# Performance work log

Hardware: AMD Instinct MI355X
Metric: run time of the kernel (lower is better)

The kernel has to match this reference:

```python
import jax, jax.numpy as jnp
import numpy as np

B, S, HD, NH, AH, F = 64, 256, 512, 8, 256, 2
DH = HD // NH          # item/pos head dim = 64
DA = AH // NH          # attribute head dim = 32
EPS = 1e-12


def setup_inputs() -> dict:
    key = jax.random.key(0)
    ks = iter(jax.random.split(key, 32))
    rn = lambda shape, s=1.0: jax.random.normal(next(ks), shape, dtype=jnp.float32) * s
    w = 0.02
    return {
        "input_tensor": rn((B, S, HD)),
        "attribute_table": rn((B, S, 1, AH)),
        "position_embedding": rn((B, S, HD)),
        "Wq": rn((HD, HD), w), "bq": jnp.zeros((HD,), jnp.float32),
        "Wk": rn((HD, HD), w), "bk": jnp.zeros((HD,), jnp.float32),
        "Wv": rn((HD, HD), w), "bv": jnp.zeros((HD,), jnp.float32),
        "Wqp": rn((HD, HD), w), "bqp": jnp.zeros((HD,), jnp.float32),
        "Wkp": rn((HD, HD), w), "bkp": jnp.zeros((HD,), jnp.float32),
        "Wqa": rn((F, AH, AH), w), "bqa": jnp.zeros((F, AH), jnp.float32),
        "Wka": rn((F, AH, AH), w), "bka": jnp.zeros((F, AH), jnp.float32),
        "fw1": rn((S, S), w), "fb1": jnp.zeros((S,), jnp.float32),
        "fw2": rn((1, S), w), "fb2": jnp.zeros((1,), jnp.float32),
        "Wd": rn((HD, HD), w), "bd": jnp.zeros((HD,), jnp.float32),
        "gamma": jnp.ones((HD,), jnp.float32),
        "beta": jnp.zeros((HD,), jnp.float32),
    }


def _split_heads(x, nh):
    b, s, h = x.shape
    return x.reshape(b, s, nh, h // nh).transpose(0, 2, 1, 3)  # [B,H,S,d]


def reference(input_tensor, attribute_table, position_embedding,
              Wq, bq, Wk, bk, Wv, bv, Wqp, bqp, Wkp, bkp,
              Wqa, bqa, Wka, bka, fw1, fb1, fw2, fb2,
              Wd, bd, gamma, beta):
    q = _split_heads(input_tensor @ Wq.T + bq, NH)
    k = _split_heads(input_tensor @ Wk.T + bk, NH)
    v = _split_heads(input_tensor @ Wv.T + bv, NH)
    qp = _split_heads(position_embedding @ Wqp.T + bqp, NH)
    kp = _split_heads(position_embedding @ Wkp.T + bkp, NH)

    item_scores = jnp.einsum('bhqd,bhkd->bhqk', q, k)
    pos_scores = jnp.einsum('bhqd,bhkd->bhqk', qp, kp)

    attr = attribute_table.squeeze(-2)                       # [B,S,AH]
    qa = jnp.einsum('bsc,foc->fbso', attr, Wqa) + bqa[:, None, None, :]
    ka = jnp.einsum('bsc,foc->fbso', attr, Wka) + bka[:, None, None, :]
    qa = qa.reshape(F, B, S, NH, DA).transpose(0, 1, 3, 2, 4)  # [F,B,H,S,da]
    ka = ka.reshape(F, B, S, NH, DA).transpose(0, 1, 3, 2, 4)
    attr_scores = jnp.einsum('fbhqd,fbhkd->fbhqk', qa, ka)
    attr_scores = attr_scores.transpose(1, 2, 3, 0, 4)         # [B,H,S,F,S]

    # gate fusion (VanillaAttention over the F+2 score sources)
    stacked = jnp.concatenate(
        [attr_scores, item_scores[..., None, :], pos_scores[..., None, :]],
        axis=-2)                                               # [B,H,S,F+2,S]
    energy = jnp.maximum(stacked @ fw1.T + fb1, 0.0) @ fw2.T + fb2
    gate_w = jax.nn.softmax(energy.squeeze(-1), axis=-1)        # [B,H,S,F+2]
    scores = jnp.sum(stacked * gate_w[..., None], axis=-2)      # [B,H,S,S]

    scores = scores / np.sqrt(DH).astype(np.float32)
    probs = jax.nn.softmax(scores, axis=-1)
    ctx = jnp.einsum('bhqk,bhkd->bhqd', probs, v)
    ctx = ctx.transpose(0, 2, 1, 3).reshape(B, S, HD)

    h = ctx @ Wd.T + bd
    x = h + input_tensor
    mu = jnp.mean(x, axis=-1, keepdims=True)
    var = jnp.mean(jnp.square(x - mu), axis=-1, keepdims=True)
    return gamma * (x - mu) / jnp.sqrt(var + EPS) + beta
```

## Files before the change

### kernel.cpp

```cpp
#include <hip/hip_runtime.h>

typedef unsigned short u16;
typedef unsigned int   u32;
typedef __bf16 bf16x8 __attribute__((ext_vector_type(8)));
typedef float  f32x4  __attribute__((ext_vector_type(4)));
typedef u16    u16x4  __attribute__((ext_vector_type(4)));
typedef u16    u16x8  __attribute__((ext_vector_type(8)));

#define BB 64
#define SS 256
#define HDIM 512
#define NHEAD 8
#define BS (BB*SS)
#define NBH 512

__device__ __forceinline__ u16 f2bf(float f){
    u32 u = __builtin_bit_cast(u32, f);
    u32 r = u + 0x7FFFu + ((u>>16)&1u);
    return (u16)(r>>16);
}
__device__ __forceinline__ float bf2f(u16 u){
    return __builtin_bit_cast(float, (u32)u<<16);
}
__device__ __forceinline__ void gload16(const void* g, void* l){
    __builtin_amdgcn_global_load_lds(
        (const __attribute__((address_space(1))) void*)g,
        (__attribute__((address_space(3))) void*)l, 16, 0, 0);
}

__device__ __forceinline__ size_t zrow(int bh, int s){
    return ((size_t)bh*256 + s)*384;
}

__global__ __launch_bounds__(256) void cvt_k(const float* __restrict__ s,
                                             u16* __restrict__ d, int n8)
{
    int i = blockIdx.x*256 + threadIdx.x;
    const int stride = gridDim.x*256;
    for (; i < n8; i += stride) {
        f32x4 a = ((const f32x4*)s)[i*2];
        f32x4 b = ((const f32x4*)s)[i*2+1];
        u16x8 o = { f2bf(a[0]),f2bf(a[1]),f2bf(a[2]),f2bf(a[3]),
                    f2bf(b[0]),f2bf(b[1]),f2bf(b[2]),f2bf(b[3]) };
        ((u16x8*)d)[i] = o;
    }
}

__global__ __launch_bounds__(256) void cvtW_k(
    const float* __restrict__ Wq,  const float* __restrict__ Wk,
    const float* __restrict__ Wv,  const float* __restrict__ Wqp,
    const float* __restrict__ Wkp, const float* __restrict__ Wqa,
    const float* __restrict__ Wka, const float* __restrict__ Wd,
    u16* __restrict__ dst)
{
    const int i = blockIdx.x*256 + threadIdx.x;
    const float* s; u16* d; int local;
    if (i < 163840) {
        const int seg = i >> 15; local = i & 32767;
        s = seg==0?Wq:seg==1?Wk:seg==2?Wv:seg==3?Wqp:Wkp;
        d = dst + (size_t)seg*262144;
    } else if (i < 196608) {
        const int j = i - 163840; const int seg = j >> 14; local = j & 16383;
        s = seg ? Wka : Wqa;
        d = dst + 1310720 + (size_t)seg*131072;
    } else {
        local = i - 196608;
        s = Wd; d = dst + 1572864;
    }
    f32x4 a = ((const f32x4*)s)[local*2];
    f32x4 b = ((const f32x4*)s)[local*2+1];
    u16x8 o = { f2bf(a[0]),f2bf(a[1]),f2bf(a[2]),f2bf(a[3]),
                f2bf(b[0]),f2bf(b[1]),f2bf(b[2]),f2bf(b[3]) };
    ((u16x8*)d)[local] = o;
}

__global__ __launch_bounds__(64) void prep_fw1(const float* __restrict__ fw1,
                                               u16* __restrict__ fw1b)
{
    const int row = blockIdx.x;
    const int c0  = threadIdx.x * 4;
    float4 v = *(const float4*)(fw1 + (size_t)row*256 + c0);
    u16x4 pk = { f2bf(v.x), f2bf(v.y), f2bf(v.z), f2bf(v.w) };
    *(u16x4*)((char*)fw1b + (size_t)row*512 + ((c0*2) ^ ((row&7)<<4))) = pk;
}

template<int OUTMODE, int BBF16>
__global__ __launch_bounds__(256,2) void gemm128(
    const u16* __restrict__ A, const void* __restrict__ Bv,
    void* __restrict__ o0, void* __restrict__ o1, void* __restrict__ o2,
    const float* __restrict__ b0, const float* __restrict__ b1,
    const float* __restrict__ b2, const float* __restrict__ resid,
    int N, int K)
{
    __shared__ char sA[16384];
    __shared__ char sB[16384];
    const int tid = threadIdx.x, lane = tid & 63, w = tid >> 6;
    const int wr = (w & 1) * 64, wc = (w >> 1) * 64;
    const int flat = blockIdx.x;
    const int xcd = flat & 7, bi2 = flat >> 3;
    const int n_i = bi2 >> 4, mIn = bi2 & 15;
    const int m0 = (xcd*16 + mIn)*128, n0 = n_i*128;

    f32x4 acc[4][4];
    #pragma unroll
    for (int mi = 0; mi < 4; mi++)
        #pragma unroll
        for (int ni = 0; ni < 4; ni++) acc[mi][ni] = (f32x4){0.f,0.f,0.f,0.f};

    for (int k0 = 0; k0 < K; k0 += 64) {
        __syncthreads();
        #pragma unroll
        for (int i = 0; i < 4; i++) {
            const int off = w*4096 + i*1024 + lane*16;
            const int r = off >> 7, c = off & 0x70;
            gload16(A + (size_t)(m0 + r)*K + k0 + ((c ^ ((r&7)<<4)) >> 1),
                    sA + w*4096 + i*1024);
        }
        if (BBF16) {
            const u16* B = (const u16*)Bv;
            #pragma unroll
            for (int i = 0; i < 4; i++) {
                const int off = w*4096 + i*1024 + lane*16;
                const int r = off >> 7, c = off & 0x70;
                gload16(B + (size_t)(n0 + r)*K + k0 + ((c ^ ((r&7)<<4)) >> 1),
                        sB + w*4096 + i*1024);
            }
        } else {
            const float* B = (const float*)Bv;
            const int r = tid >> 1, cseg = (tid & 1) * 32;
            const float* p = B + (size_t)(n0 + r)*K + k0 + cseg;
            alignas(16) u16 tmp[32];
            #pragma unroll
            for (int j = 0; j < 8; j++) {
                float4 fv = ((const float4*)p)[j];
                tmp[j*4+0]=f2bf(fv.x); tmp[j*4+1]=f2bf(fv.y);
                tmp[j*4+2]=f2bf(fv.z); tmp[j*4+3]=f2bf(fv.w);
            }
            const int rx = (r&7)<<4;
            #pragma unroll
            for (int j = 0; j < 4; j++)
                *(u16x8*)(sB + r*128 + ((cseg*2 + j*16) ^ rx)) = *(u16x8*)(tmp + j*8);
        }
        __syncthreads();
        bf16x8 af[2][4], bf[2][4];
        #pragma unroll
        for (int ks = 0; ks < 2; ks++) {
            const int kb = ks*64 + (lane>>4)*16;
            #pragma unroll
            for (int mi = 0; mi < 4; mi++) {
                const int r = wr + mi*16 + (lane&15);
                af[ks][mi] = *(const bf16x8*)(sA + r*128 + (kb ^ ((r&7)<<4)));
            }
            #pragma unroll
            for (int ni = 0; ni < 4; ni++) {
                const int r = wc + ni*16 + (lane&15);
                bf[ks][ni] = *(const bf16x8*)(sB + r*128 + (kb ^ ((r&7)<<4)));
            }
        }
        #pragma unroll
        for (int ks = 0; ks < 2; ks++)
            #pragma unroll
            for (int mi = 0; mi < 4; mi++)
                #pragma unroll
                for (int ni = 0; ni < 4; ni++)
                    acc[mi][ni] = __builtin_amdgcn_mfma_f32_16x16x32_bf16(
                        af[ks][mi], bf[ks][ni], acc[mi][ni], 0,0,0);
    }
    #pragma unroll
    for (int mi = 0; mi < 4; mi++) {
        const int rowb = m0 + wr + mi*16 + (lane>>4)*4;
        const int bi = rowb >> 8, s0 = rowb & 255;
        #pragma unroll
        for (int ni = 0; ni < 4; ni++) {
            const int gn = n0 + wc + ni*16 + (lane&15);
            if (OUTMODE == 2) {
                float* out = (float*)o0;
                const float bb = b0[gn];
                #pragma unroll
                for (int r = 0; r < 4; r++) {
                    size_t idx = (size_t)(rowb+r)*N + gn;
                    out[idx] = acc[mi][ni][r] + bb + resid[idx];
                }
            } else if (OUTMODE == 4) {
                const int seg = gn >> 9, o = gn & 511;
                const int hh = o >> 6, d = o & 63;
                const float bb = (seg==0?b0:seg==1?b1:b2)[o];
                const int bh = bi*8 + hh;
                if (seg < 2) {
                    char* outp = (char*)(seg ? o1 : o0);
                    #pragma unroll
                    for (int r = 0; r < 4; r++) {
                        const int s = s0 + r;
                        *(u16*)(outp + zrow(bh,s) + ((d*2) ^ ((s&7)<<4)))
                            = f2bf(acc[mi][ni][r] + bb);
                    }
                } else {
                    u16x4 pk;
                    #pragma unroll
                    for (int r = 0; r < 4; r++) pk[r] = f2bf(acc[mi][ni][r] + bb);
                    *(u16x4*)((char*)o2 + (size_t)bh*32768 + d*512
                                        + ((s0*2) ^ ((d&7)<<4))) = pk;
                }
            } else if (OUTMODE == 5) {
                const int seg = gn >> 9, o = gn & 511;
                const int hh = o >> 6, d = o & 63;
                const float bb = (seg ? b1 : b0)[o];
                const int bh = bi*8 + hh;
                char* outp = (char*)(seg ? o1 : o0);
                #pragma unroll
                for (int r = 0; r < 4; r++) {
                    const int s = s0 + r;
                    *(u16*)(outp + zrow(bh,s) + (((64+d)*2) ^ ((s&7)<<4)))
                        = f2bf(acc[mi][ni][r] + bb);
                }
            } else {
                const int qk = gn >> 9, fo = gn & 511;
                const int f = fo >> 8, o = fo & 255;
                const int hh = o >> 5, d = o & 31;
                const int cb = 128 + f*32;
                const float bb = (qk ? b1 : b0)[fo];
                const int bh = bi*8 + hh;
                char* outp = (char*)(qk ? o1 : o0);
                #pragma unroll
                for (int r = 0; r < 4; r++) {
                    const int s = s0 + r;
                    *(u16*)(outp + zrow(bh,s) + (((cb+d)*2) ^ ((s&7)<<4)))
                        = f2bf(acc[mi][ni][r] + bb);
                }
            }
        }
    }
}

#define QZ34  98304
#define SM34  122880

__global__ __launch_bounds__(1024,1) void k34(
    const u16* __restrict__ QZ, const u16* __restrict__ KZ,
    const u16* __restrict__ fw1b, const float* __restrict__ fb1,
    const float* __restrict__ fw2, float* __restrict__ e)
{
    extern __shared__ char sm[];
    const int tid = threadIdx.x, lane = tid & 63, w = tid >> 6;
    const int bh = blockIdx.x;
    const int l15 = lane & 15, lq = lane >> 4;

    {
        const int s = tid & 255, dg = tid >> 8;
        const char* rowp = (const char*)KZ + zrow(bh, s);
        const int sw = (s & 7) << 4;
        #pragma unroll
        for (int m = 0; m < 6; m++) {
            const int d0 = dg*48 + m*8;
            u16x8 v = *(const u16x8*)(rowp + ((d0*2) ^ sw));
            #pragma unroll
            for (int ee = 0; ee < 8; ee++) {
                const int d = d0 + ee;
                *(u16*)(sm + d*512 + ((s*2) ^ ((d&7)<<4))) = v[ee];
            }
        }
    }
    __syncthreads();

    const int ar  = w*16 + l15;
    const int asw = (l15 & 7) << 4;
    f32x4 kacc[12];
    #pragma unroll
    for (int ni = 0; ni < 12; ni++) kacc[ni] = (f32x4){0.f,0.f,0.f,0.f};
    #pragma unroll
    for (int ks = 0; ks < 8; ks++) {
        const int kb = ks*64 + lq*16;
        bf16x8 a = *(const bf16x8*)((const char*)fw1b + (size_t)ar*512 + (kb ^ asw));
        #pragma unroll
        for (int ni = 0; ni < 12; ni++) {
            const int dr = ni*16 + l15;
            bf16x8 b = *(const bf16x8*)(sm + dr*512 + (kb ^ ((dr&7)<<4)));
            kacc[ni] = __builtin_amdgcn_mfma_f32_16x16x32_bf16(a, b, kacc[ni], 0,0,0);
        }
    }
    __syncthreads();

    #pragma unroll
    for (int ni = 0; ni < 12; ni++) {
        const int d = ni*16 + l15;
        #pragma unroll
        for (int r = 0; r < 4; r++) {
            const int jl = w*16 + lq*4 + r;
            *(u16*)(sm + jl*384 + ((d*2) ^ ((jl&7)<<4))) = f2bf(kacc[ni][r]);
        }
    }
    bf16x8 af2[6];
    #pragma unroll
    for (int ks = 0; ks < 6; ks++)
        af2[ks] = *(const bf16x8*)(sm + ar*384 + ((ks*64 + lq*16) ^ asw));

    float f1v[4], f2v[4];
    #pragma unroll
    for (int r = 0; r < 4; r++) {
        const int j = w*16 + lq*4 + r;
        f1v[r] = fb1[j]; f2v[r] = fw2[j];
    }
    __syncthreads();

    for (int qt = 0; qt < 4; qt++) {
        __syncthreads();
        gload16((const char*)QZ + zrow(bh, qt*64) + w*1024 + lane*16,
                sm + QZ34 + w*1024);
        if (w < 8)
            gload16((const char*)QZ + zrow(bh, qt*64) + 16384 + w*1024 + lane*16,
                    sm + QZ34 + 16384 + w*1024);
        __syncthreads();
        #pragma unroll
        for (int half = 0; half < 2; half++) {
            f32x4 acc[4][2];
            #pragma unroll
            for (int s = 0; s < 4; s++)
                #pragma unroll
                for (int n2 = 0; n2 < 2; n2++) acc[s][n2] = (f32x4){0.f,0.f,0.f,0.f};
            #pragma unroll
            for (int ks = 0; ks < 6; ks++) {
                const int sidx = (ks<2)?0:(ks<4)?1:(ks<5)?2:3;
                const int kb = ks*64 + lq*16;
                #pragma unroll
                for (int n2 = 0; n2 < 2; n2++) {
                    const int qr = (half*2 + n2)*16 + l15;
                    bf16x8 b = *(const bf16x8*)(sm + QZ34 + qr*384 + (kb ^ ((qr&7)<<4)));
                    acc[sidx][n2] = __builtin_amdgcn_mfma_f32_16x16x32_bf16(
                        af2[ks], b, acc[sidx][n2], 0,0,0);
                }
            }
            #pragma unroll
            for (int src = 0; src < 4; src++)
                #pragma unroll
                for (int n2 = 0; n2 < 2; n2++) {
                    float ep = 0.f;
                    #pragma unroll
                    for (int r = 0; r < 4; r++)
                        ep += fmaxf(acc[src][n2][r] + f1v[r], 0.f) * f2v[r];
                    ep += __shfl_xor(ep, 16);
                    ep += __shfl_xor(ep, 32);
                    if (lane < 16)
                        ((float*)sm)[w*1024 + src*256 + qt*64 + (half*2+n2)*16 + lane] = ep;
                }
        }
    }
    __syncthreads();
    {
        const int q = tid & 255, src = tid >> 8;
        const float* el = (const float*)sm;
        float s = 0.f;
        #pragma unroll
        for (int w2 = 0; w2 < 16; w2++) s += el[w2*1024 + src*256 + q];
        e[((size_t)bh*256 + q)*4 + src] = s;
    }
}

#define K5_KZ 24576
#define K5_VT 49152
#define K5_SMEM 81920

__global__ __launch_bounds__(256,2) void k5_mix(
    const u16* __restrict__ QZ, const u16* __restrict__ KZ,
    const u16* __restrict__ VT, const float* __restrict__ e,
    u16* __restrict__ ctx)
{
    extern __shared__ char sm[];
    const int tid = threadIdx.x, lane = tid & 63, w = tid >> 6;
    const int flat = blockIdx.x;
    const int xcd = flat & 7, idx = flat >> 3;
    const int qt = idx & 3;
    const int bh = (idx >> 2) * 8 + xcd;
    const int q0 = qt*64;
    const int b = bh >> 3, h = bh & 7;
    const int kq16 = (lane>>4)*16;

    #pragma unroll
    for (int i = 0; i < 6; i++)
        gload16((const char*)QZ + zrow(bh, q0) + i*4096 + w*1024 + lane*16,
                sm + i*4096 + w*1024);
    #pragma unroll
    for (int i = 0; i < 8; i++)
        gload16((const char*)VT + (size_t)bh*32768 + i*4096 + w*1024 + lane*16,
                sm + K5_VT + i*4096 + w*1024);
    #pragma unroll
    for (int i = 0; i < 6; i++)
        gload16((const char*)KZ + zrow(bh, 0) + i*4096 + w*1024 + lane*16,
                sm + K5_KZ + i*4096 + w*1024);
    __syncthreads();

    const int qrow = w*16 + (lane&15);
    float ga[4];
    {
        f32x4 ev = *(const f32x4*)(e + ((size_t)bh*256 + q0 + qrow)*4);
        float em = fmaxf(fmaxf(ev[0],ev[1]), fmaxf(ev[2],ev[3]));
        float s = 0.f;
        #pragma unroll
        for (int j = 0; j < 4; j++) { ga[j] = __expf(ev[j]-em); s += ga[j]; }
        const float gi = 1.f / s;
        #pragma unroll
        for (int j = 0; j < 4; j++) ga[j] *= gi;
    }
    const int asw = ((lane&15)&7) << 4;
    bf16x8 aF[6];
    #pragma unroll
    for (int ks = 0; ks < 6; ks++) {
        const int sidx = (ks<2)?0:(ks<4)?1:(ks<5)?2:3;
        u16x8 v = *(const u16x8*)(sm + qrow*384 + ((ks*64 + kq16) ^ asw));
        const float gg = ga[sidx];
        u16x8 pk;
        #pragma unroll
        for (int j = 0; j < 8; j++) pk[j] = f2bf(bf2f(v[j]) * gg);
        aF[ks] = __builtin_bit_cast(bf16x8, pk);
    }

    f32x4 macc[4][4];
    #pragma unroll
    for (int kt = 0; kt < 4; kt++)
        #pragma unroll
        for (int n = 0; n < 4; n++) macc[kt][n] = (f32x4){0.f,0.f,0.f,0.f};
    u16x8 kreg[6];
    #pragma unroll
    for (int kt = 0; kt < 4; kt++) {
        if (kt < 3) {
            #pragma unroll
            for (int j = 0; j < 6; j++)
                kreg[j] = *(const u16x8*)((const char*)KZ + zrow(bh, (kt+1)*64)
                                          + (tid + j*256)*16);
        }
        #pragma unroll
        for (int n = 0; n < 4; n++) {
            const int kr = n*16 + (lane&15);
            const int ksw = (kr&7)<<4;
            #pragma unroll
            for (int ks = 0; ks < 6; ks++) {
                bf16x8 bb = *(const bf16x8*)(sm + K5_KZ + kr*384 + ((ks*64 + kq16) ^ ksw));
                macc[kt][n] = __builtin_amdgcn_mfma_f32_16x16x32_bf16(
                    aF[ks], bb, macc[kt][n], 0,0,0);
            }
        }
        if (kt < 3) {
            __syncthreads();
            #pragma unroll
            for (int j = 0; j < 6; j++)
                *(u16x8*)(sm + K5_KZ + (tid + j*256)*16) = kreg[j];
            __syncthreads();
        }
    }
    __syncthreads();

    #pragma unroll
    for (int rr = 0; rr < 4; rr++) {
        float mx = -3.4e38f;
        #pragma unroll
        for (int kt = 0; kt < 4; kt++)
            #pragma unroll
            for (int n = 0; n < 4; n++) mx = fmaxf(mx, macc[kt][n][rr]);
        #pragma unroll
        for (int msk = 1; msk < 16; msk <<= 1) mx = fmaxf(mx, __shfl_xor(mx, msk));
        float s = 0.f;
        #pragma unroll
        for (int kt = 0; kt < 4; kt++)
            #pragma unroll
            for (int n = 0; n < 4; n++) {
                float pv = __expf((macc[kt][n][rr] - mx) * 0.125f);
                macc[kt][n][rr] = pv; s += pv;
            }
        #pragma unroll
        for (int msk = 1; msk < 16; msk <<= 1) s += __shfl_xor(s, msk);
        const float inv = 1.f / s;
        const int orow = w*16 + (lane>>4)*4 + rr;
        const int osw = (orow&7)<<4;
        #pragma unroll
        for (int kt = 0; kt < 4; kt++)
            #pragma unroll
            for (int n = 0; n < 4; n++) {
                const int col = kt*64 + n*16 + (lane&15);
                *(u16*)(sm + orow*512 + ((col*2) ^ osw)) = f2bf(macc[kt][n][rr]*inv);
            }
    }
    __syncthreads();

    f32x4 pacc[4];
    #pragma unroll
    for (int n = 0; n < 4; n++) pacc[n] = (f32x4){0.f,0.f,0.f,0.f};
    const int prow = w*16 + (lane&15);
    const int psw = ((lane&15)&7)<<4;
    #pragma unroll
    for (int ks = 0; ks < 8; ks++) {
        const int kb = ks*64 + kq16;
        bf16x8 a = *(const bf16x8*)(sm + prow*512 + (kb ^ psw));
        #pragma unroll
        for (int n = 0; n < 4; n++) {
            const int dr = n*16 + (lane&15);
            bf16x8 bb = *(const bf16x8*)(sm + K5_VT + dr*512 + (kb ^ ((dr&7)<<4)));
            pacc[n] = __builtin_amdgcn_mfma_f32_16x16x32_bf16(a, bb, pacc[n], 0,0,0);
        }
    }
    {
        const int orow = w*16 + (lane>>4)*4;
        #pragma unroll
        for (int n = 0; n < 4; n++) {
            const int d = n*16 + (lane&15);
            #pragma unroll
            for (int r = 0; r < 4; r++) {
                const size_t grow = (size_t)b*256 + q0 + orow + r;
                ctx[grow*512 + h*64 + d] = f2bf(pacc[n][r]);
            }
        }
    }
}

__global__ __launch_bounds__(256) void ln_k(float* __restrict__ x,
    const float* __restrict__ gamma, const float* __restrict__ beta)
{
    const int row = blockIdx.x*4 + (threadIdx.x >> 6);
    const int l = threadIdx.x & 63;
    float* p = x + (size_t)row*HDIM;
    f32x4 v0 = *(const f32x4*)(p + l*4);
    f32x4 v1 = *(const f32x4*)(p + 256 + l*4);
    float s = v0[0]+v0[1]+v0[2]+v0[3] + v1[0]+v1[1]+v1[2]+v1[3];
    #pragma unroll
    for (int msk = 1; msk < 64; msk <<= 1) s += __shfl_xor(s, msk);
    const float mu = s * (1.f/512.f);
    float vs = 0.f;
    #pragma unroll
    for (int j = 0; j < 4; j++) {
        float d0 = v0[j]-mu, d1 = v1[j]-mu;
        vs += d0*d0 + d1*d1;
    }
    #pragma unroll
    for (int msk = 1; msk < 64; msk <<= 1) vs += __shfl_xor(vs, msk);
    const float inv = 1.f / sqrtf(vs * (1.f/512.f) + 1e-12f);
    f32x4 o0, o1;
    #pragma unroll
    for (int j = 0; j < 4; j++) {
        o0[j] = gamma[l*4+j]     * (v0[j]-mu) * inv + beta[l*4+j];
        o1[j] = gamma[256+l*4+j] * (v1[j]-mu) * inv + beta[256+l*4+j];
    }
    *(f32x4*)(p + l*4) = o0;
    *(f32x4*)(p + 256 + l*4) = o1;
}

extern "C" void kernel_launch(void* const* d_in, const int* in_sizes, int n_in,
                              void* d_out, int out_size, void* d_ws, size_t ws_size,
                              hipStream_t stream)
{
    const float* input = (const float*)d_in[0];
    const float* attrt = (const float*)d_in[1];
    const float* pose  = (const float*)d_in[2];
    const float* Wq  = (const float*)d_in[3];  const float* bq  = (const float*)d_in[4];
    const float* Wk  = (const float*)d_in[5];  const float* bk  = (const float*)d_in[6];
    const float* Wv  = (const float*)d_in[7];  const float* bv  = (const float*)d_in[8];
    const float* Wqp = (const float*)d_in[9];  const float* bqp = (const float*)d_in[10];
    const float* Wkp = (const float*)d_in[11]; const float* bkp = (const float*)d_in[12];
    const float* Wqa = (const float*)d_in[13]; const float* bqa = (const float*)d_in[14];
    const float* Wka = (const float*)d_in[15]; const float* bka = (const float*)d_in[16];
    const float* fw1 = (const float*)d_in[17]; const float* fb1 = (const float*)d_in[18];
    const float* fw2 = (const float*)d_in[19];
    const float* Wd  = (const float*)d_in[21]; const float* bd  = (const float*)d_in[22];
    const float* gamma = (const float*)d_in[23]; const float* beta = (const float*)d_in[24];

    char* ws = (char*)d_ws;
    u16*   wsQZ  = (u16*)(ws);
    u16*   wsKZ  = (u16*)(ws + 50331648);
    u16*   wsTmp = (u16*)(ws + 100663296);
    float* wsE   = (float*)(ws + 117440512);
    u16*   fw1b  = (u16*)(ws + 119537664);
    u16*   dW    = (u16*)(ws + 119668736);
    u16*   wsVT  = (u16*)d_out;

    dim3 blk(256);

    cvtW_k<<<dim3(896), blk, 0, stream>>>(Wq, Wk, Wv, Wqp, Wkp, Wqa, Wka, Wd, dW);
    prep_fw1<<<dim3(256), dim3(64), 0, stream>>>(fw1, fw1b);

    cvt_k<<<dim3(2048), blk, 0, stream>>>(attrt, wsTmp, 524288);
    gemm128<6,1><<<dim3(1024), blk, 0, stream>>>(wsTmp, dW + 1310720,
        wsQZ, wsKZ, nullptr, bqa, bka, nullptr, nullptr, 1024, 256);
    cvt_k<<<dim3(2048), blk, 0, stream>>>(input, wsTmp, 1048576);
    gemm128<4,1><<<dim3(1536), blk, 0, stream>>>(wsTmp, dW,
        wsQZ, wsKZ, wsVT, bq, bk, bv, nullptr, 1536, 512);
    cvt_k<<<dim3(2048), blk, 0, stream>>>(pose, wsTmp, 1048576);
    gemm128<5,1><<<dim3(1024), blk, 0, stream>>>(wsTmp, dW + 786432,
        wsQZ, wsKZ, nullptr, bqp, bkp, nullptr, nullptr, 1024, 512);

    hipFuncSetAttribute(reinterpret_cast<const void*>(k34),
                        hipFuncAttributeMaxDynamicSharedMemorySize, SM34);
    k34<<<dim3(NBH), dim3(1024), SM34, stream>>>(wsQZ, wsKZ, fw1b, fb1, fw2, wsE);

    hipFuncSetAttribute(reinterpret_cast<const void*>(k5_mix),
                        hipFuncAttributeMaxDynamicSharedMemorySize, K5_SMEM);
    k5_mix<<<dim3(2048), blk, K5_SMEM, stream>>>(wsQZ, wsKZ, wsVT, wsE, wsTmp);

    gemm128<2,1><<<dim3(512), blk, 0, stream>>>(wsTmp, dW + 1572864,
        d_out, nullptr, nullptr, bd, nullptr, nullptr, input, 512, 512);
    ln_k<<<dim3(BS/4), blk, 0, stream>>>((float*)d_out, gamma, beta);
}
```

Before: 252.8 us.

## Split gate-energy kernel per head into two half-source blocks with double-buffered Q staging

```diff
diff --git a/kernel.cpp b/kernel.cpp
--- a/kernel.cpp
+++ b/kernel.cpp
@@ -232,126 +232,190 @@
     }
 }
 
-#define QZ34  98304
-#define SM34  122880
-
-__global__ __launch_bounds__(1024,1) void k34(
+#define K34B_QZ   53248
+#define K34B_QZSZ 13312
+#define K34B_SMEM (53248 + 2*13312)
+
+__global__ __launch_bounds__(512,4) void k34b(
     const u16* __restrict__ QZ, const u16* __restrict__ KZ,
     const u16* __restrict__ fw1b, const float* __restrict__ fb1,
     const float* __restrict__ fw2, float* __restrict__ e)
 {
     extern __shared__ char sm[];
     const int tid = threadIdx.x, lane = tid & 63, w = tid >> 6;
-    const int bh = blockIdx.x;
+    const int bh = blockIdx.x >> 1, sp = blockIdx.x & 1;
     const int l15 = lane & 15, lq = lane >> 4;
-
+    const int base0 = sp ? 64 : 0;
+    const int base1 = sp ? 160 : 128;
+
+    auto stage_qz = [&](int qt4, int buf) {
+        char* dst = sm + K34B_QZ + buf*K34B_QZSZ;
+        {
+            const int li = w*64 + lane;
+            const int q = li / 13, c = li - q*13;
+            const int cc = (c == 12) ? 0 : c;
+            const int ld = cc*8;
+            const int gd = (ld < 64) ? base0 + ld : base1 + (ld - 64);
+            gload16((const char*)QZ + zrow(bh, qt4*64 + q)
+                        + ((gd*2) ^ ((q&7)<<4)),
+                    dst + w*1024);
+        }
+        if (w < 5) {
+            const int li = 512 + w*64 + lane;
+            const int q = li / 13, c = li - q*13;
+            const int cc = (c == 12) ? 0 : c;
+            const int ld = cc*8;
+            const int gd = (ld < 64) ? base0 + ld : base1 + (ld - 64);
+            gload16((const char*)QZ + zrow(bh, qt4*64 + q)
+                        + ((gd*2) ^ ((q&7)<<4)),
+                    dst + 8192 + w*1024);
+        }
+    };
+
+    stage_qz(0, 0);
     {
-        const int s = tid & 255, dg = tid >> 8;
-        const char* rowp = (const char*)KZ + zrow(bh, s);
-        const int sw = (s & 7) << 4;
-        #pragma unroll
-        for (int m = 0; m < 6; m++) {
-            const int d0 = dg*48 + m*8;
-            u16x8 v = *(const u16x8*)(rowp + ((d0*2) ^ sw));
+        const int spair = tid & 127, dg = tid >> 7;
+        const int s0 = spair*2;
+        const char* r0 = (const char*)KZ + zrow(bh, s0);
+        const char* r1 = (const char*)KZ + zrow(bh, s0+1);
+        const int sw0 = (s0&7)<<4, sw1 = ((s0+1)&7)<<4;
+        #pragma unroll
+        for (int m = 0; m < 3; m++) {
+            const int ld0 = dg*24 + m*8;
+            const int gd = (ld0 < 64) ? base0 + ld0 : base1 + (ld0 - 64);
+            u16x8 v0 = *(const u16x8*)(r0 + ((gd*2) ^ sw0));
+            u16x8 v1 = *(const u16x8*)(r1 + ((gd*2) ^ sw1));
             #pragma unroll
             for (int ee = 0; ee < 8; ee++) {
-                const int d = d0 + ee;
-                *(u16*)(sm + d*512 + ((s*2) ^ ((d&7)<<4))) = v[ee];
+                const int d = ld0 + ee;
+                *(u32*)(sm + d*512 + ((s0*2) ^ ((d&7)<<4)))
+                    = (u32)v0[ee] | ((u32)v1[ee] << 16);
             }
         }
     }
     __syncthreads();
 
-    const int ar  = w*16 + l15;
-    const int asw = (l15 & 7) << 4;
-    f32x4 kacc[12];
-    #pragma unroll
-    for (int ni = 0; ni < 12; ni++) kacc[ni] = (f32x4){0.f,0.f,0.f,0.f};
+    const int jb = w & 3, dh = w >> 2;
+    f32x4 kacc[4][3];
+    #pragma unroll
+    for (int js = 0; js < 4; js++)
+        #pragma unroll
+        for (int ni = 0; ni < 3; ni++) kacc[js][ni] = (f32x4){0.f,0.f,0.f,0.f};
     #pragma unroll
     for (int ks = 0; ks < 8; ks++) {
         const int kb = ks*64 + lq*16;
-        bf16x8 a = *(const bf16x8*)((const char*)fw1b + (size_t)ar*512 + (kb ^ asw));
-        #pragma unroll
-        for (int ni = 0; ni < 12; ni++) {
-            const int dr = ni*16 + l15;
+        bf16x8 a[4];
+        #pragma unroll
+        for (int js = 0; js < 4; js++) {
+            const int ar = jb*64 + js*16 + l15;
+            a[js] = *(const bf16x8*)((const char*)fw1b + (size_t)ar*512
+                                     + (kb ^ ((l15&7)<<4)));
+        }
+        #pragma unroll
+        for (int ni = 0; ni < 3; ni++) {
+            const int dr = dh*48 + ni*16 + l15;
             bf16x8 b = *(const bf16x8*)(sm + dr*512 + (kb ^ ((dr&7)<<4)));
-            kacc[ni] = __builtin_amdgcn_mfma_f32_16x16x32_bf16(a, b, kacc[ni], 0,0,0);
+            #pragma unroll
+            for (int js = 0; js < 4; js++)
+                kacc[js][ni] = __builtin_amdgcn_mfma_f32_16x16x32_bf16(
+                    a[js], b, kacc[js][ni], 0,0,0);
         }
     }
     __syncthreads();
 
     #pragma unroll
-    for (int ni = 0; ni < 12; ni++) {
-        const int d = ni*16 + l15;
+    for (int js = 0; js < 4; js++)
+        #pragma unroll
+        for (int ni = 0; ni < 3; ni++) {
+            const int d = dh*48 + ni*16 + l15;
+            #pragma unroll
+            for (int r = 0; r < 4; r++) {
+                const int j = jb*64 + js*16 + lq*4 + r;
+                *(u16*)(sm + j*208 + d*2) = f2bf(kacc[js][ni][r]);
+            }
+        }
+    __syncthreads();
+
+    const int qh = w >> 2;
+    bf16x8 af2[4][3];
+    #pragma unroll
+    for (int js = 0; js < 4; js++) {
+        const int ar = jb*64 + js*16 + l15;
+        #pragma unroll
+        for (int ks = 0; ks < 3; ks++)
+            af2[js][ks] = *(const bf16x8*)(sm + ar*208 + ks*64 + lq*16);
+    }
+    float f1v[4][4], f2v[4][4];
+    #pragma unroll
+    for (int js = 0; js < 4; js++)
         #pragma unroll
         for (int r = 0; r < 4; r++) {
-            const int jl = w*16 + lq*4 + r;
-            *(u16*)(sm + jl*384 + ((d*2) ^ ((jl&7)<<4))) = f2bf(kacc[ni][r]);
-        }
-    }
-    bf16x8 af2[6];
-    #pragma unroll
-    for (int ks = 0; ks < 6; ks++)
-        af2[ks] = *(const bf16x8*)(sm + ar*384 + ((ks*64 + lq*16) ^ asw));
-
-    float f1v[4], f2v[4];
-    #pragma unroll
-    for (int r = 0; r < 4; r++) {
-        const int j = w*16 + lq*4 + r;
-        f1v[r] = fb1[j]; f2v[r] = fw2[j];
-    }
-    __syncthreads();
+            const int j = jb*64 + js*16 + lq*4 + r;
+            f1v[js][r] = fb1[j]; f2v[js][r] = fw2[j];
+        }
 
     for (int qt = 0; qt < 4; qt++) {
         __syncthreads();
-        gload16((const char*)QZ + zrow(bh, qt*64) + w*1024 + lane*16,
-                sm + QZ34 + w*1024);
-        if (w < 8)
-            gload16((const char*)QZ + zrow(bh, qt*64) + 16384 + w*1024 + lane*16,
-                    sm + QZ34 + 16384 + w*1024);
-        __syncthreads();
-        #pragma unroll
-        for (int half = 0; half < 2; half++) {
-            f32x4 acc[4][2];
-            #pragma unroll
-            for (int s = 0; s < 4; s++)
-                #pragma unroll
-                for (int n2 = 0; n2 < 2; n2++) acc[s][n2] = (f32x4){0.f,0.f,0.f,0.f};
-            #pragma unroll
-            for (int ks = 0; ks < 6; ks++) {
-                const int sidx = (ks<2)?0:(ks<4)?1:(ks<5)?2:3;
-                const int kb = ks*64 + lq*16;
-                #pragma unroll
-                for (int n2 = 0; n2 < 2; n2++) {
-                    const int qr = (half*2 + n2)*16 + l15;
-                    bf16x8 b = *(const bf16x8*)(sm + QZ34 + qr*384 + (kb ^ ((qr&7)<<4)));
-                    acc[sidx][n2] = __builtin_amdgcn_mfma_f32_16x16x32_bf16(
-                        af2[ks], b, acc[sidx][n2], 0,0,0);
-                }
-            }
-            #pragma unroll
-            for (int src = 0; src < 4; src++)
-                #pragma unroll
-                for (int n2 = 0; n2 < 2; n2++) {
-                    float ep = 0.f;
+        if (qt < 3) stage_qz(qt+1, (qt+1)&1);
+        const char* qb = sm + K34B_QZ + (qt&1)*K34B_QZSZ;
+        #pragma unroll
+        for (int qs = 0; qs < 2; qs++) {
+            const int qoff = (qh*32 + qs*16 + l15)*208 + lq*16;
+            f32x4 acc[4];
+            #pragma unroll
+            for (int js = 0; js < 4; js++) acc[js] = (f32x4){0.f,0.f,0.f,0.f};
+            #pragma unroll
+            for (int kk = 0; kk < 2; kk++) {
+                bf16x8 b = *(const bf16x8*)(qb + qoff + kk*64);
+                #pragma unroll
+                for (int js = 0; js < 4; js++)
+                    acc[js] = __builtin_amdgcn_mfma_f32_16x16x32_bf16(
+                        af2[js][kk], b, acc[js], 0,0,0);
+            }
+            {
+                float ep = 0.f;
+                #pragma unroll
+                for (int js = 0; js < 4; js++)
                     #pragma unroll
                     for (int r = 0; r < 4; r++)
-                        ep += fmaxf(acc[src][n2][r] + f1v[r], 0.f) * f2v[r];
-                    ep += __shfl_xor(ep, 16);
-                    ep += __shfl_xor(ep, 32);
-                    if (lane < 16)
-                        ((float*)sm)[w*1024 + src*256 + qt*64 + (half*2+n2)*16 + lane] = ep;
-                }
+                        ep += fmaxf(acc[js][r] + f1v[js][r], 0.f) * f2v[js][r];
+                ep += __shfl_xor(ep, 16);
+                ep += __shfl_xor(ep, 32);
+                if (lane < 16)
+                    ((float*)sm)[(jb*2 + 0)*256 + qt*64 + qh*32 + qs*16 + lane] = ep;
+            }
+            #pragma unroll
+            for (int js = 0; js < 4; js++) acc[js] = (f32x4){0.f,0.f,0.f,0.f};
+            {
+                bf16x8 b = *(const bf16x8*)(qb + qoff + 128);
+                #pragma unroll
+                for (int js = 0; js < 4; js++)
+                    acc[js] = __builtin_amdgcn_mfma_f32_16x16x32_bf16(
+                        af2[js][2], b, acc[js], 0,0,0);
+            }
+            {
+                float ep = 0.f;
+                #pragma unroll
+                for (int js = 0; js < 4; js++)
+                    #pragma unroll
+                    for (int r = 0; r < 4; r++)
+                        ep += fmaxf(acc[js][r] + f1v[js][r], 0.f) * f2v[js][r];
+                ep += __shfl_xor(ep, 16);
+                ep += __shfl_xor(ep, 32);
+                if (lane < 16)
+                    ((float*)sm)[(jb*2 + 1)*256 + qt*64 + qh*32 + qs*16 + lane] = ep;
+            }
         }
     }
     __syncthreads();
     {
-        const int q = tid & 255, src = tid >> 8;
+        const int q = tid & 255, sl = tid >> 8;
         const float* el = (const float*)sm;
         float s = 0.f;
         #pragma unroll
-        for (int w2 = 0; w2 < 16; w2++) s += el[w2*1024 + src*256 + q];
-        e[((size_t)bh*256 + q)*4 + src] = s;
+        for (int j2 = 0; j2 < 4; j2++) s += el[(j2*2 + sl)*256 + q];
+        const int gsrc = sl ? (2 + sp) : sp;
+        e[((size_t)bh*256 + q)*4 + gsrc] = s;
     }
 }
 
@@ -584,9 +648,9 @@
     gemm128<5,1><<<dim3(1024), blk, 0, stream>>>(wsTmp, dW + 786432,
         wsQZ, wsKZ, nullptr, bqp, bkp, nullptr, nullptr, 1024, 512);
 
-    hipFuncSetAttribute(reinterpret_cast<const void*>(k34),
-                        hipFuncAttributeMaxDynamicSharedMemorySize, SM34);
-    k34<<<dim3(NBH), dim3(1024), SM34, stream>>>(wsQZ, wsKZ, fw1b, fb1, fw2, wsE);
+    hipFuncSetAttribute(reinterpret_cast<const void*>(k34b),
+                        hipFuncAttributeMaxDynamicSharedMemorySize, K34B_SMEM);
+    k34b<<<dim3(NBH*2), dim3(512), K34B_SMEM, stream>>>(wsQZ, wsKZ, fw1b, fb1, fw2, wsE);
 
     hipFuncSetAttribute(reinterpret_cast<const void*>(k5_mix),
                         hipFuncAttributeMaxDynamicSharedMemorySize, K5_SMEM);
```

After: 238.5 us. 5.6% less time.
